# Kernel optimization log

Measured on AMD Instinct MI355X. Metric: run time of the kernel, lower is better.

The kernel has to match this reference:

```python
import jax, jax.numpy as jnp
import numpy as np

B = 512
EPS = 1e-5


def _coords():
    # cvt_coord(i) = [(i//5 - 2)/2, (i%5 - 2)/2] on a 5x5 grid
    c = np.array([[(i // 5 - 2) / 2.0, (i % 5 - 2) / 2.0] for i in range(25)], dtype=np.float32)
    return jnp.asarray(c)  # [25, 2]


def setup_inputs() -> dict:
    key = jax.random.key(0)
    ks = jax.random.split(key, 32)
    d = {
        'img': jax.random.normal(ks[0], (B, 3, 75, 75), jnp.float32),
        'qst': jax.random.normal(ks[1], (B, 11), jnp.float32),
    }
    # conv backbone params
    cin = [3, 24, 24, 24]
    for l in range(4):
        d[f'conv_w{l+1}'] = jax.random.normal(ks[2 + l], (24, cin[l], 3, 3), jnp.float32) * 0.1
        d[f'conv_b{l+1}'] = jnp.zeros((24,), jnp.float32)
        d[f'bn_g{l+1}'] = 1.0 + 0.05 * jax.random.normal(ks[6 + l], (24,), jnp.float32)
        d[f'bn_b{l+1}'] = 0.05 * jax.random.normal(ks[10 + l], (24,), jnp.float32)
    # g MLP (63->256, 256->256 x3)
    d['g_w1'] = jax.random.normal(ks[14], (256, 63), jnp.float32) * 0.05
    d['g_b1'] = jnp.zeros((256,), jnp.float32)
    for l in (2, 3, 4):
        d[f'g_w{l}'] = jax.random.normal(ks[13 + l], (256, 256), jnp.float32) * 0.05
        d[f'g_b{l}'] = jnp.zeros((256,), jnp.float32)
    # f MLP and output head
    d['f_w1'] = jax.random.normal(ks[20], (256, 256), jnp.float32) * 0.05
    d['f_b1'] = jnp.zeros((256,), jnp.float32)
    d['fc2_w'] = jax.random.normal(ks[21], (256, 256), jnp.float32) * 0.05
    d['fc2_b'] = jnp.zeros((256,), jnp.float32)
    d['fc3_w'] = jax.random.normal(ks[22], (10, 256), jnp.float32) * 0.05
    d['fc3_b'] = jnp.zeros((10,), jnp.float32)
    return d


def _conv_bn(x, w, b, g, be):
    y = jax.lax.conv_general_dilated(x, w, (2, 2), [(1, 1), (1, 1)],
                                     dimension_numbers=('NCHW', 'OIHW', 'NCHW'))
    y = jax.nn.relu(y + b[None, :, None, None])
    # BatchNorm2d with batch statistics (training-mode forward)
    mu = jnp.mean(y, axis=(0, 2, 3), keepdims=True)
    var = jnp.var(y, axis=(0, 2, 3), keepdims=True)
    return (y - mu) * jax.lax.rsqrt(var + EPS) * g[None, :, None, None] + be[None, :, None, None]


def _lin(x, w, b):
    return x @ w.T + b


def reference(img, qst,
              conv_w1, conv_b1, bn_g1, bn_b1,
              conv_w2, conv_b2, bn_g2, bn_b2,
              conv_w3, conv_b3, bn_g3, bn_b3,
              conv_w4, conv_b4, bn_g4, bn_b4,
              g_w1, g_b1, g_w2, g_b2, g_w3, g_b3, g_w4, g_b4,
              f_w1, f_b1, fc2_w, fc2_b, fc3_w, fc3_b):
    x = _conv_bn(img, conv_w1, conv_b1, bn_g1, bn_b1)
    x = _conv_bn(x, conv_w2, conv_b2, bn_g2, bn_b2)
    x = _conv_bn(x, conv_w3, conv_b3, bn_g3, bn_b3)
    x = _conv_bn(x, conv_w4, conv_b4, bn_g4, bn_b4)  # [B, 24, 5, 5]
    mb = x.shape[0]
    x_flat = x.reshape(mb, 24, 25).transpose(0, 2, 1)  # [B, 25, 24]
    coords = jnp.broadcast_to(_coords()[None], (mb, 25, 2))
    x_flat = jnp.concatenate([x_flat, coords], axis=2)  # [B, 25, 26]
    # all-pairs: pair (p, q) -> concat(obj_q, obj_p, qst)
    xj = jnp.concatenate([x_flat, jnp.broadcast_to(qst[:, None, :], (mb, 25, 11))], axis=2)  # [B,25,37]
    x_i = jnp.broadcast_to(x_flat[:, None, :, :], (mb, 25, 25, 26))
    x_j = jnp.broadcast_to(xj[:, :, None, :], (mb, 25, 25, 37))
    x_full = jnp.concatenate([x_i, x_j], axis=3).reshape(mb * 625, 63)
    h = jax.nn.relu(_lin(x_full, g_w1, g_b1))
    h = jax.nn.relu(_lin(h, g_w2, g_b2))
    h = jax.nn.relu(_lin(h, g_w3, g_b3))
    h = jax.nn.relu(_lin(h, g_w4, g_b4))
    x_g = h.reshape(mb, 625, 256).sum(axis=1)  # [B, 256]
    x_f = jax.nn.relu(_lin(x_g, f_w1, f_b1))
    x_f = jax.nn.relu(_lin(x_f, fc2_w, fc2_b))  # (dropout omitted: eval/deterministic)
    logits = _lin(x_f, fc3_w, fc3_b)
    return jax.nn.log_softmax(logits, axis=-1)
```

## Files before the change

### kernel.cpp

```cpp
#include <hip/hip_runtime.h>
#include <hip/hip_bf16.h>

#define EPS 1e-5f

typedef _Float16 half_t;
typedef __attribute__((ext_vector_type(8))) _Float16 h16x8;
typedef __attribute__((ext_vector_type(4))) _Float16 h16x4;
typedef __attribute__((ext_vector_type(4))) float f32x4;

__device__ __forceinline__ float relu_f(float x) { return x > 0.f ? x : 0.f; }

#define OFF_Y1   0
#define OFF_Y2   17743872
#define OFF_Y3   22179840
#define OFF_Y4   23408640
#define OFF_ST   23715840
#define OFF_WHL  23718912
#define OFF_A    0
#define OFF_BV   3276800
#define OFF_XG   6553600

__global__ __launch_bounds__(256) void k_prep(const float* w2, const float* w3,
                                              const float* w4, half_t* whl, float* stats) {
    int idx = blockIdx.x * 256 + threadIdx.x;
    if (idx < 3072) stats[idx] = 0.f;
    int l = idx >> 16, e = idx & 65535;
    const float* w = (l == 0) ? w2 : (l == 1) ? w3 : w4;
    float v = w[e];
    int c = e >> 8, k = e & 255;
    int o = ((c >> 4) * 8 + (k >> 5)) * 512 + ((k >> 3) & 3) * 128 + (c & 15) * 8 + (k & 7);
    whl[l * 65536 + o] = (half_t)v;
}

__global__ __launch_bounds__(256, 2) void k_conv1(const float* img, const float* w,
                                                  const float* bias, half_t* y1, float* ostats) {
    __shared__ float wl[648], bl[24], red[4][48];
    int tid = threadIdx.x;
    if (tid < 24) bl[tid] = bias[tid];
    for (int i = tid; i < 648; i += 256) wl[i] = w[i];
    __syncthreads();
    int idx = blockIdx.x * 256 + tid;
    int b2 = idx / 1444, rem = idx % 1444;
    int b0 = b2 * 2;
    int oh = rem / 38, ow = rem % 38;
    float acc0[24], acc1[24];
#pragma unroll
    for (int o = 0; o < 24; ++o) { acc0[o] = bl[o]; acc1[o] = bl[o]; }
    for (int ic = 0; ic < 3; ++ic) {
        float p0[9], p1[9];
#pragma unroll
        for (int kh = 0; kh < 3; ++kh) {
            int ih = oh * 2 - 1 + kh;
#pragma unroll
            for (int kw = 0; kw < 3; ++kw) {
                int iw = ow * 2 - 1 + kw;
                bool ok = (unsigned)ih < 75u && (unsigned)iw < 75u;
                p0[kh * 3 + kw] = ok ? img[((b0 * 3 + ic) * 75 + ih) * 75 + iw] : 0.f;
                p1[kh * 3 + kw] = ok ? img[(((b0 + 1) * 3 + ic) * 75 + ih) * 75 + iw] : 0.f;
            }
        }
#pragma unroll
        for (int o = 0; o < 24; ++o)
#pragma unroll
            for (int t = 0; t < 9; ++t) {
                float wv = wl[(o * 3 + ic) * 9 + t];
                acc0[o] += wv * p0[t];
                acc1[o] += wv * p1[t];
            }
    }
#pragma unroll
    for (int o = 0; o < 24; ++o) { acc0[o] = relu_f(acc0[o]); acc1[o] = relu_f(acc1[o]); }
#pragma unroll
    for (int g = 0; g < 3; ++g) {
        h16x8 a, c;
#pragma unroll
        for (int j = 0; j < 8; ++j) { a[j] = (half_t)acc0[g * 8 + j]; c[j] = (half_t)acc1[g * 8 + j]; }
        *(h16x8*)&y1[((long)(b0) * 1444 + rem) * 24 + g * 8] = a;
        *(h16x8*)&y1[((long)(b0 + 1) * 1444 + rem) * 24 + g * 8] = c;
    }
    int wave = tid >> 6;
#pragma unroll
    for (int o = 0; o < 24; ++o) {
        float v = acc0[o] + acc1[o];
        float v2 = acc0[o] * acc0[o] + acc1[o] * acc1[o];
#pragma unroll
        for (int off = 1; off < 64; off <<= 1) { v += __shfl_xor(v, off); v2 += __shfl_xor(v2, off); }
        if ((tid & 63) == 0) { red[wave][o] = v; red[wave][24 + o] = v2; }
    }
    __syncthreads();
    if (tid < 48)
        atomicAdd(&ostats[(blockIdx.x & 15) * 48 + tid],
                  red[0][tid] + red[1][tid] + red[2][tid] + red[3][tid]);
}

__global__ __launch_bounds__(256) void k_conv2(const half_t* yin, const float* w,
                                               const float* bias, const float* instats,
                                               const float* bng, const float* bnb,
                                               float* yout, float* ostats) {
    __shared__ float wl[5184], bl[24], scs[24], shs[24], red[4][48];
    int tid = threadIdx.x;
    if (tid < 24) {
        float s = 0.f, s2 = 0.f;
#pragma unroll
        for (int k = 0; k < 16; ++k) { s += instats[k * 48 + tid]; s2 += instats[k * 48 + 24 + tid]; }
        float mu = s * (1.f / 739328.f);
        float var = s2 * (1.f / 739328.f) - mu * mu;
        float sca = bng[tid] * rsqrtf(var + EPS);
        scs[tid] = sca; shs[tid] = bnb[tid] - mu * sca;
        bl[tid] = bias[tid];
    }
    for (int i = tid; i < 5184; i += 256) {
        int t = i / 576, r = i % 576;
        int o = r / 24, ic = r % 24;
        wl[i] = w[(o * 24 + ic) * 9 + t];
    }
    __syncthreads();
    int idx = blockIdx.x * 256 + tid;
    int b2 = idx / 361, rem = idx % 361;
    int b0 = b2 * 2;
    int oh = rem / 19, ow = rem % 19;
    float acc0[24], acc1[24];
#pragma unroll
    for (int o = 0; o < 24; ++o) { acc0[o] = bl[o]; acc1[o] = bl[o]; }
#pragma unroll
    for (int kh = 0; kh < 3; ++kh) {
        int ih = oh * 2 - 1 + kh;
#pragma unroll
        for (int kw = 0; kw < 3; ++kw) {
            int iw = ow * 2 - 1 + kw;
            if ((unsigned)ih < 38u && (unsigned)iw < 38u) {
                long px = (long)ih * 38 + iw;
                const half_t* s0 = &yin[((long)b0 * 1444 + px) * 24];
                const half_t* s1 = &yin[((long)(b0 + 1) * 1444 + px) * 24];
                const float* wt = &wl[(kh * 3 + kw) * 576];
#pragma unroll
                for (int g = 0; g < 3; ++g) {
                    h16x8 v0 = *(const h16x8*)&s0[g * 8];
                    h16x8 v1 = *(const h16x8*)&s1[g * 8];
                    float p0[8], p1[8];
#pragma unroll
                    for (int j = 0; j < 8; ++j) {
                        float sc = scs[g * 8 + j], sh = shs[g * 8 + j];
                        p0[j] = (float)v0[j] * sc + sh;
                        p1[j] = (float)v1[j] * sc + sh;
                    }
#pragma unroll
                    for (int o = 0; o < 24; ++o) {
                        const float4* w4 = (const float4*)&wt[o * 24 + g * 8];
                        float4 wa = w4[0], wb = w4[1];
                        acc0[o] += wa.x * p0[0] + wa.y * p0[1] + wa.z * p0[2] + wa.w * p0[3]
                                 + wb.x * p0[4] + wb.y * p0[5] + wb.z * p0[6] + wb.w * p0[7];
                        acc1[o] += wa.x * p1[0] + wa.y * p1[1] + wa.z * p1[2] + wa.w * p1[3]
                                 + wb.x * p1[4] + wb.y * p1[5] + wb.z * p1[6] + wb.w * p1[7];
                    }
                }
            }
        }
    }
    int wave = tid >> 6;
#pragma unroll
    for (int o = 0; o < 24; ++o) {
        acc0[o] = relu_f(acc0[o]);
        acc1[o] = relu_f(acc1[o]);
        yout[(b0 * 24 + o) * 361 + rem] = acc0[o];
        yout[((b0 + 1) * 24 + o) * 361 + rem] = acc1[o];
        float v = acc0[o] + acc1[o];
        float v2 = acc0[o] * acc0[o] + acc1[o] * acc1[o];
#pragma unroll
        for (int off = 1; off < 64; off <<= 1) { v += __shfl_xor(v, off); v2 += __shfl_xor(v2, off); }
        if ((tid & 63) == 0) { red[wave][o] = v; red[wave][24 + o] = v2; }
    }
    __syncthreads();
    if (tid < 48)
        atomicAdd(&ostats[(blockIdx.x & 15) * 48 + tid],
                  red[0][tid] + red[1][tid] + red[2][tid] + red[3][tid]);
}

__global__ __launch_bounds__(256) void k_conv(const float* yin, const float* w,
                                              const float* bias, const float* instats,
                                              const float* bng, const float* bnb,
                                              float* yout, float* ostats,
                                              int Hin, int Hout, float invN) {
    __shared__ float wl[5184], bl[24], sc[24], sh[24], red[4][48];
    int tid = threadIdx.x;
    if (tid < 24) {
        float s = 0.f, s2 = 0.f;
#pragma unroll
        for (int k = 0; k < 16; ++k) { s += instats[k * 48 + tid]; s2 += instats[k * 48 + 24 + tid]; }
        float mu = s * invN;
        float var = s2 * invN - mu * mu;
        float sca = bng[tid] * rsqrtf(var + EPS);
        sc[tid] = sca; sh[tid] = bnb[tid] - mu * sca;
        bl[tid] = bias[tid];
    }
    for (int i = tid; i < 5184; i += 256) wl[i] = w[i];
    __syncthreads();
    int idx = blockIdx.x * 256 + tid;
    int HWo = Hout * Hout;
    int b = idx / HWo, rem = idx % HWo;
    int oh = rem / Hout, ow = rem % Hout;
    float acc[24];
#pragma unroll
    for (int o = 0; o < 24; ++o) acc[o] = bl[o];
    for (int ic = 0; ic < 24; ++ic) {
        float patch[9];
        float scc = sc[ic], shc = sh[ic];
#pragma unroll
        for (int kh = 0; kh < 3; ++kh) {
            int ih = oh * 2 - 1 + kh;
#pragma unroll
            for (int kw = 0; kw < 3; ++kw) {
                int iw = ow * 2 - 1 + kw;
                bool ok = (unsigned)ih < (unsigned)Hin && (unsigned)iw < (unsigned)Hin;
                patch[kh * 3 + kw] = ok ? yin[((b * 24 + ic) * Hin + ih) * Hin + iw] * scc + shc : 0.f;
            }
        }
#pragma unroll
        for (int o = 0; o < 24; ++o)
#pragma unroll
            for (int t = 0; t < 9; ++t) acc[o] += wl[(o * 24 + ic) * 9 + t] * patch[t];
    }
    int wave = tid >> 6;
#pragma unroll
    for (int o = 0; o < 24; ++o) {
        acc[o] = relu_f(acc[o]);
        yout[(b * 24 + o) * HWo + rem] = acc[o];
        float v = acc[o], v2 = v * v;
#pragma unroll
        for (int off = 1; off < 64; off <<= 1) { v += __shfl_xor(v, off); v2 += __shfl_xor(v2, off); }
        if ((tid & 63) == 0) { red[wave][o] = v; red[wave][24 + o] = v2; }
    }
    __syncthreads();
    if (tid < 48)
        atomicAdd(&ostats[(blockIdx.x & 15) * 48 + tid],
                  red[0][tid] + red[1][tid] + red[2][tid] + red[3][tid]);
}

__global__ __launch_bounds__(256) void k_obj(const float* y4, const float* qst,
                                             const float* w1, const float* b1,
                                             const float* instats, const float* bng,
                                             const float* bnb, float* A, float* Bv, float* xg) {
    int b = blockIdx.x, tid = threadIdx.x;
    __shared__ float w1l[16128];
    __shared__ float objs[25][28];
    __shared__ float sc[24], sh[24], q[11];
    xg[b * 256 + tid] = 0.f;
    for (int i = tid; i < 16128; i += 256) w1l[i] = w1[i];
    if (tid < 24) {
        float s = 0.f, s2 = 0.f;
#pragma unroll
        for (int k = 0; k < 16; ++k) { s += instats[k * 48 + tid]; s2 += instats[k * 48 + 24 + tid]; }
        float mu = s * (1.f / 12800.f);
        float var = s2 * (1.f / 12800.f) - mu * mu;
        float sca = bng[tid] * rsqrtf(var + EPS);
        sc[tid] = sca; sh[tid] = bnb[tid] - mu * sca;
    }
    if (tid < 11) q[tid] = qst[b * 11 + tid];
    __syncthreads();
    for (int i = tid; i < 600; i += 256) {
        int c = i / 25, p = i % 25;
        objs[p][c] = y4[b * 600 + i] * sc[c] + sh[c];
    }
    if (tid < 25) { objs[tid][24] = ((tid / 5) - 2) * 0.5f; objs[tid][25] = ((tid % 5) - 2) * 0.5f; }
    __syncthreads();
    float wr[63];
#pragma unroll
    for (int k = 0; k < 63; ++k) wr[k] = w1l[tid * 63 + k];
    float qdot = b1[tid];
#pragma unroll
    for (int j = 0; j < 11; ++j) qdot += wr[52 + j] * q[j];
#pragma unroll 1
    for (int p = 0; p < 25; ++p) {
        float a = 0.f, bv = qdot;
#pragma unroll
        for (int k = 0; k < 26; ++k) { a += wr[k] * objs[p][k]; bv += wr[26 + k] * objs[p][k]; }
        A[(b * 25 + p) * 256 + tid] = a;
        Bv[(b * 25 + p) * 256 + tid] = bv;
    }
}

__global__ __launch_bounds__(256, 4) void k_g(const float* A, const float* Bv, const half_t* whl,
                                              const float* gb2, const float* gb3,
                                              const float* gb4, float* xg) {
    __shared__ alignas(16) half_t h[64 * 264];
    __shared__ float biasL[3][256];
    int tid = threadIdx.x;
    int lb = (blockIdx.x & 7) * 640 + (blockIdx.x >> 3);
    int b = lb / 10, t = lb % 10;
    int r0 = t * 64;
    int rmax = 625 - r0; if (rmax > 64) rmax = 64;
    biasL[0][tid] = gb2[tid];
    biasL[1][tid] = gb3[tid];
    biasL[2][tid] = gb4[tid];
    const float* Ab = A + b * 6400;
    const float* Bb = Bv + b * 6400;
#pragma unroll
    for (int it = 0; it < 16; ++it) {
        int r = it * 4 + (tid >> 6);
        int rs = __builtin_amdgcn_readfirstlane(r);
        int pr = r0 + rs; if (pr > 624) pr = 624;
        int i = pr % 25, j = pr / 25;
        int c4 = (tid & 63) << 2;
        float4 av = *(const float4*)&Ab[i * 256 + c4];
        float4 bv = *(const float4*)&Bb[j * 256 + c4];
        h16x4 hv = {(half_t)relu_f(av.x + bv.x), (half_t)relu_f(av.y + bv.y),
                    (half_t)relu_f(av.z + bv.z), (half_t)relu_f(av.w + bv.w)};
        *(h16x4*)&h[r * 264 + c4] = hv;
    }
    __syncthreads();
    int cg = tid >> 6, lane = tid & 63;
    int quad = lane >> 4, l15 = lane & 15;
    const half_t* hr = h + l15 * 264;
    const half_t* Wl = whl + (cg * 4) * 8 * 512 + lane * 8;
#pragma unroll 1
    for (int layer = 0; layer < 3; ++layer) {
        const half_t* W = Wl + layer * 65536;
        f32x4 acc[4][4];
#pragma unroll
        for (int mi = 0; mi < 4; ++mi)
#pragma unroll
            for (int nt = 0; nt < 4; ++nt) acc[mi][nt] = (f32x4){0.f, 0.f, 0.f, 0.f};
        h16x8 aw0 = *(const h16x8*)&W[0 * 4096];
        h16x8 aw1 = *(const h16x8*)&W[1 * 4096];
        h16x8 aw2 = *(const h16x8*)&W[2 * 4096];
        h16x8 aw3 = *(const h16x8*)&W[3 * 4096];
        h16x8 bh0 = *(const h16x8*)&hr[0 * 4224 + quad * 8];
        h16x8 bh1 = *(const h16x8*)&hr[1 * 4224 + quad * 8];
#pragma unroll 2
        for (int ks = 0; ks < 8; ++ks) {
            int ko = ks * 32 + quad * 8;
            int ksn = (ks + 1) & 7;
            int kon = ksn * 32 + quad * 8;
            h16x8 bh2 = *(const h16x8*)&hr[2 * 4224 + ko];
            h16x8 bh3 = *(const h16x8*)&hr[3 * 4224 + ko];
            h16x8 an0 = *(const h16x8*)&W[0 * 4096 + ksn * 512];
            h16x8 an1 = *(const h16x8*)&W[1 * 4096 + ksn * 512];
            h16x8 an2 = *(const h16x8*)&W[2 * 4096 + ksn * 512];
            h16x8 an3 = *(const h16x8*)&W[3 * 4096 + ksn * 512];
            __builtin_amdgcn_s_setprio(1);
            acc[0][0] = __builtin_amdgcn_mfma_f32_16x16x32_f16(aw0, bh0, acc[0][0], 0, 0, 0);
            acc[1][0] = __builtin_amdgcn_mfma_f32_16x16x32_f16(aw1, bh0, acc[1][0], 0, 0, 0);
            acc[2][0] = __builtin_amdgcn_mfma_f32_16x16x32_f16(aw2, bh0, acc[2][0], 0, 0, 0);
            acc[3][0] = __builtin_amdgcn_mfma_f32_16x16x32_f16(aw3, bh0, acc[3][0], 0, 0, 0);
            acc[0][1] = __builtin_amdgcn_mfma_f32_16x16x32_f16(aw0, bh1, acc[0][1], 0, 0, 0);
            acc[1][1] = __builtin_amdgcn_mfma_f32_16x16x32_f16(aw1, bh1, acc[1][1], 0, 0, 0);
            acc[2][1] = __builtin_amdgcn_mfma_f32_16x16x32_f16(aw2, bh1, acc[2][1], 0, 0, 0);
            acc[3][1] = __builtin_amdgcn_mfma_f32_16x16x32_f16(aw3, bh1, acc[3][1], 0, 0, 0);
            h16x8 bn0 = *(const h16x8*)&hr[0 * 4224 + kon];
            h16x8 bn1 = *(const h16x8*)&hr[1 * 4224 + kon];
            acc[0][2] = __builtin_amdgcn_mfma_f32_16x16x32_f16(aw0, bh2, acc[0][2], 0, 0, 0);
            acc[1][2] = __builtin_amdgcn_mfma_f32_16x16x32_f16(aw1, bh2, acc[1][2], 0, 0, 0);
            acc[2][2] = __builtin_amdgcn_mfma_f32_16x16x32_f16(aw2, bh2, acc[2][2], 0, 0, 0);
            acc[3][2] = __builtin_amdgcn_mfma_f32_16x16x32_f16(aw3, bh2, acc[3][2], 0, 0, 0);
            acc[0][3] = __builtin_amdgcn_mfma_f32_16x16x32_f16(aw0, bh3, acc[0][3], 0, 0, 0);
            acc[1][3] = __builtin_amdgcn_mfma_f32_16x16x32_f16(aw1, bh3, acc[1][3], 0, 0, 0);
            acc[2][3] = __builtin_amdgcn_mfma_f32_16x16x32_f16(aw2, bh3, acc[2][3], 0, 0, 0);
            acc[3][3] = __builtin_amdgcn_mfma_f32_16x16x32_f16(aw3, bh3, acc[3][3], 0, 0, 0);
            __builtin_amdgcn_s_setprio(0);
            aw0 = an0; aw1 = an1; aw2 = an2; aw3 = an3;
            bh0 = bn0; bh1 = bn1;
        }
        __syncthreads();
        if (layer < 2) {
#pragma unroll
            for (int mi = 0; mi < 4; ++mi) {
                int c0 = cg * 64 + mi * 16 + quad * 4;
#pragma unroll
                for (int nt = 0; nt < 4; ++nt) {
                    int row = nt * 16 + l15;
                    h16x4 hv;
#pragma unroll
                    for (int v = 0; v < 4; ++v)
                        hv[v] = (half_t)relu_f(acc[mi][nt][v] + biasL[layer][c0 + v]);
                    *(h16x4*)&h[row * 264 + c0] = hv;
                }
            }
            __syncthreads();
        } else {
#pragma unroll
            for (int mi = 0; mi < 4; ++mi) {
                int c0 = cg * 64 + mi * 16 + quad * 4;
#pragma unroll
                for (int v = 0; v < 4; ++v) {
                    float s = 0.f;
#pragma unroll
                    for (int nt = 0; nt < 4; ++nt) {
                        int row = nt * 16 + l15;
                        float x = relu_f(acc[mi][nt][v] + biasL[2][c0 + v]);
                        if (row < rmax) s += x;
                    }
                    s += __shfl_xor(s, 1);
                    s += __shfl_xor(s, 2);
                    s += __shfl_xor(s, 4);
                    s += __shfl_xor(s, 8);
                    if (l15 == 0) atomicAdd(&xg[b * 256 + c0 + v], s);
                }
            }
        }
    }
}

__global__ __launch_bounds__(256) void k_f(const float* xg, const float* fw1, const float* fb1,
                                           const float* fw2, const float* fb2,
                                           const float* fw3, const float* fb3, float* out) {
    int b0 = blockIdx.x * 2, tid = threadIdx.x;
    __shared__ float xb[2][256], h1[2][256], l10[2][10], red[2];
    xb[0][tid] = xg[b0 * 256 + tid];
    xb[1][tid] = xg[(b0 + 1) * 256 + tid];
    __syncthreads();
    float s0 = fb1[tid], s1 = s0;
    {
        const float4* wr = (const float4*)&fw1[tid * 256];
        const float4* x0 = (const float4*)xb[0];
        const float4* x1 = (const float4*)xb[1];
#pragma unroll 8
        for (int k = 0; k < 64; ++k) {
            float4 w = wr[k], a = x0[k], c = x1[k];
            s0 += w.x * a.x + w.y * a.y + w.z * a.z + w.w * a.w;
            s1 += w.x * c.x + w.y * c.y + w.z * c.z + w.w * c.w;
        }
    }
    h1[0][tid] = relu_f(s0);
    h1[1][tid] = relu_f(s1);
    __syncthreads();
    s0 = fb2[tid]; s1 = s0;
    {
        const float4* wr = (const float4*)&fw2[tid * 256];
        const float4* x0 = (const float4*)h1[0];
        const float4* x1 = (const float4*)h1[1];
#pragma unroll 8
        for (int k = 0; k < 64; ++k) {
            float4 w = wr[k], a = x0[k], c = x1[k];
            s0 += w.x * a.x + w.y * a.y + w.z * a.z + w.w * a.w;
            s1 += w.x * c.x + w.y * c.y + w.z * c.z + w.w * c.w;
        }
    }
    __syncthreads();
    xb[0][tid] = relu_f(s0);
    xb[1][tid] = relu_f(s1);
    __syncthreads();
    if (tid < 20) {
        int bb = tid / 10, o = tid % 10;
        float v = fb3[o];
        const float4* wr = (const float4*)&fw3[o * 256];
        const float4* hv = (const float4*)xb[bb];
#pragma unroll 8
        for (int k = 0; k < 64; ++k) {
            float4 w = wr[k], x = hv[k];
            v += w.x * x.x + w.y * x.y + w.z * x.z + w.w * x.w;
        }
        l10[bb][o] = v;
    }
    __syncthreads();
    if (tid < 2) {
        float m = l10[tid][0];
        for (int i = 1; i < 10; ++i) m = fmaxf(m, l10[tid][i]);
        float e = 0.f;
        for (int i = 0; i < 10; ++i) e += expf(l10[tid][i] - m);
        red[tid] = m + logf(e);
    }
    __syncthreads();
    if (tid < 20) {
        int bb = tid / 10, o = tid % 10;
        out[(b0 + bb) * 10 + o] = l10[bb][o] - red[bb];
    }
}

extern "C" void kernel_launch(void* const* d_in, const int* in_sizes, int n_in,
                              void* d_out, int out_size, void* d_ws, size_t ws_size,
                              hipStream_t stream) {
    const float* img = (const float*)d_in[0];
    const float* qst = (const float*)d_in[1];
    const float* cw[4] = {(const float*)d_in[2], (const float*)d_in[6],
                          (const float*)d_in[10], (const float*)d_in[14]};
    const float* cb[4] = {(const float*)d_in[3], (const float*)d_in[7],
                          (const float*)d_in[11], (const float*)d_in[15]};
    const float* bg[4] = {(const float*)d_in[4], (const float*)d_in[8],
                          (const float*)d_in[12], (const float*)d_in[16]};
    const float* bb[4] = {(const float*)d_in[5], (const float*)d_in[9],
                          (const float*)d_in[13], (const float*)d_in[17]};
    const float* gw1 = (const float*)d_in[18];
    const float* gb1 = (const float*)d_in[19];
    const float* gw2 = (const float*)d_in[20];
    const float* gb2 = (const float*)d_in[21];
    const float* gw3 = (const float*)d_in[22];
    const float* gb3 = (const float*)d_in[23];
    const float* gw4 = (const float*)d_in[24];
    const float* gb4 = (const float*)d_in[25];
    const float* fw1 = (const float*)d_in[26];
    const float* fb1 = (const float*)d_in[27];
    const float* fw2 = (const float*)d_in[28];
    const float* fb2 = (const float*)d_in[29];
    const float* fw3 = (const float*)d_in[30];
    const float* fb3 = (const float*)d_in[31];

    float* ws = (float*)d_ws;
    half_t* y1 = (half_t*)(ws + OFF_Y1);
    float* y2 = ws + OFF_Y2;
    float* y3 = ws + OFF_Y3;
    float* y4 = ws + OFF_Y4;
    float* st = ws + OFF_ST;
    half_t* whl = (half_t*)(ws + OFF_WHL);
    float* A = ws + OFF_A;
    float* Bv = ws + OFF_BV;
    float* xg = ws + OFF_XG;
    float* out = (float*)d_out;

    k_prep<<<768, 256, 0, stream>>>(gw2, gw3, gw4, whl, st);
    k_conv1<<<1444, 256, 0, stream>>>(img, cw[0], cb[0], y1, st + 0 * 768);
    k_conv2<<<361, 256, 0, stream>>>(y1, cw[1], cb[1], st + 0 * 768, bg[0], bb[0], y2,
                                     st + 1 * 768);
    k_conv<<<200, 256, 0, stream>>>(y2, cw[2], cb[2], st + 1 * 768, bg[1], bb[1], y3,
                                    st + 2 * 768, 19, 10, 1.f / 184832.f);
    k_conv<<<50, 256, 0, stream>>>(y3, cw[3], cb[3], st + 2 * 768, bg[2], bb[2], y4,
                                   st + 3 * 768, 10, 5, 1.f / 51200.f);
    k_obj<<<512, 256, 0, stream>>>(y4, qst, gw1, gb1, st + 3 * 768, bg[3], bb[3], A, Bv, xg);
    k_g<<<5120, 256, 0, stream>>>(A, Bv, whl, gb2, gb3, gb4, xg);
    k_f<<<256, 256, 0, stream>>>(xg, fw1, fb1, fw2, fb2, fw3, fb3, out);
}
```

Measured before the change: 583.2 us.

## Rewrite conv2 as per-image implicit GEMM on MFMA with LDS-staged input

```diff
diff --git a/kernel.cpp b/kernel.cpp
--- a/kernel.cpp
+++ b/kernel.cpp
@@ -19,6 +19,7 @@
 #define OFF_A    0
 #define OFF_BV   3276800
 #define OFF_XG   6553600
+#define OFF_WHL2 8871936
 
 __global__ __launch_bounds__(256) void k_prep(const float* w2, const float* w3,
                                               const float* w4, half_t* whl, float* stats) {
@@ -32,6 +33,21 @@
     whl[l * 65536 + o] = (half_t)v;
 }
 
+__global__ __launch_bounds__(256) void k_prep2(const float* w2, half_t* whl2) {
+    int idx = blockIdx.x * 256 + threadIdx.x;
+    int ntile = idx / 3584, r = idx % 3584;
+    int ks = r / 512, w = r % 512;
+    int quad = w / 128, l15 = (w >> 3) & 15, j = w & 7;
+    int k = ks * 32 + quad * 8 + j;
+    int oc = ntile * 16 + l15;
+    float v = 0.f;
+    if (k < 216 && oc < 24) {
+        int tap = k / 24, ic = k % 24;
+        v = w2[(oc * 24 + ic) * 9 + tap];
+    }
+    whl2[idx] = (half_t)v;
+}
+
 __global__ __launch_bounds__(256, 2) void k_conv1(const float* img, const float* w,
                                                   const float* bias, half_t* y1, float* ostats) {
     __shared__ float wl[648], bl[24], red[4][48];
@@ -93,12 +109,16 @@
                   red[0][tid] + red[1][tid] + red[2][tid] + red[3][tid]);
 }
 
-__global__ __launch_bounds__(256) void k_conv2(const half_t* yin, const float* w,
+__global__ __launch_bounds__(256) void k_conv2(const half_t* yin, const half_t* whl2,
                                                const float* bias, const float* instats,
                                                const float* bng, const float* bnb,
                                                float* yout, float* ostats) {
-    __shared__ float wl[5184], bl[24], scs[24], shs[24], red[4][48];
+    __shared__ half_t yL[34672];
+    __shared__ half_t wf[7168];
+    __shared__ float outL[8856];
+    __shared__ float scs[24], shs[24], bl[24], red[4][48];
     int tid = threadIdx.x;
+    int b = blockIdx.x;
     if (tid < 24) {
         float s = 0.f, s2 = 0.f;
 #pragma unroll
@@ -109,68 +129,75 @@
         scs[tid] = sca; shs[tid] = bnb[tid] - mu * sca;
         bl[tid] = bias[tid];
     }
-    for (int i = tid; i < 5184; i += 256) {
-        int t = i / 576, r = i % 576;
-        int o = r / 24, ic = r % 24;
-        wl[i] = w[(o * 24 + ic) * 9 + t];
-    }
-    __syncthreads();
-    int idx = blockIdx.x * 256 + tid;
-    int b2 = idx / 361, rem = idx % 361;
-    int b0 = b2 * 2;
-    int oh = rem / 19, ow = rem % 19;
-    float acc0[24], acc1[24];
-#pragma unroll
-    for (int o = 0; o < 24; ++o) { acc0[o] = bl[o]; acc1[o] = bl[o]; }
-#pragma unroll
-    for (int kh = 0; kh < 3; ++kh) {
-        int ih = oh * 2 - 1 + kh;
-#pragma unroll
-        for (int kw = 0; kw < 3; ++kw) {
-            int iw = ow * 2 - 1 + kw;
-            if ((unsigned)ih < 38u && (unsigned)iw < 38u) {
-                long px = (long)ih * 38 + iw;
-                const half_t* s0 = &yin[((long)b0 * 1444 + px) * 24];
-                const half_t* s1 = &yin[((long)(b0 + 1) * 1444 + px) * 24];
-                const float* wt = &wl[(kh * 3 + kw) * 576];
-#pragma unroll
-                for (int g = 0; g < 3; ++g) {
-                    h16x8 v0 = *(const h16x8*)&s0[g * 8];
-                    h16x8 v1 = *(const h16x8*)&s1[g * 8];
-                    float p0[8], p1[8];
-#pragma unroll
-                    for (int j = 0; j < 8; ++j) {
-                        float sc = scs[g * 8 + j], sh = shs[g * 8 + j];
-                        p0[j] = (float)v0[j] * sc + sh;
-                        p1[j] = (float)v1[j] * sc + sh;
-                    }
-#pragma unroll
-                    for (int o = 0; o < 24; ++o) {
-                        const float4* w4 = (const float4*)&wt[o * 24 + g * 8];
-                        float4 wa = w4[0], wb = w4[1];
-                        acc0[o] += wa.x * p0[0] + wa.y * p0[1] + wa.z * p0[2] + wa.w * p0[3]
-                                 + wb.x * p0[4] + wb.y * p0[5] + wb.z * p0[6] + wb.w * p0[7];
-                        acc1[o] += wa.x * p1[0] + wa.y * p1[1] + wa.z * p1[2] + wa.w * p1[3]
-                                 + wb.x * p1[4] + wb.y * p1[5] + wb.z * p1[6] + wb.w * p1[7];
-                    }
-                }
+    if (tid < 16) yL[34656 + tid] = (half_t)0.f;
+    for (int i = tid; i < 896; i += 256)
+        ((h16x8*)wf)[i] = ((const h16x8*)whl2)[i];
+    __syncthreads();
+    const half_t* ybase = yin + (long)b * 34656;
+    for (int i = tid; i < 4332; i += 256) {
+        h16x8 v = *(const h16x8*)&ybase[i * 8];
+        int ch0 = (i % 3) * 8;
+        h16x8 o;
+#pragma unroll
+        for (int j = 0; j < 8; ++j)
+            o[j] = (half_t)((float)v[j] * scs[ch0 + j] + shs[ch0 + j]);
+        *(h16x8*)&yL[i * 8] = o;
+    }
+    __syncthreads();
+    int wv = tid >> 6, lane = tid & 63, quad = lane >> 4, l15 = lane & 15;
+    float bb0 = bl[l15];
+    float bb1 = (l15 < 8) ? bl[16 + l15] : 0.f;
+    float s0 = 0.f, q0 = 0.f, s1 = 0.f, q1 = 0.f;
+    int t0 = wv * 6, t1 = t0 + 6; if (t1 > 23) t1 = 23;
+#pragma unroll 1
+    for (int t = t0; t < t1; ++t) {
+        int px0 = t * 16;
+        int pxa = px0 + l15; if (pxa > 360) pxa = 360;
+        int oh = pxa / 19, ow = pxa % 19;
+        f32x4 a0 = (f32x4){0.f, 0.f, 0.f, 0.f};
+        f32x4 a1 = (f32x4){0.f, 0.f, 0.f, 0.f};
+#pragma unroll
+        for (int ks = 0; ks < 7; ++ks) {
+            int k0 = ks * 32 + quad * 8;
+            int tap = k0 / 24, ic0 = k0 - tap * 24;
+            int kh = tap / 3, kw = tap - kh * 3;
+            int ih = oh * 2 - 1 + kh, iw = ow * 2 - 1 + kw;
+            bool val = (tap < 9) && ((unsigned)ih < 38u) && ((unsigned)iw < 38u);
+            int aoff = val ? ((ih * 38 + iw) * 24 + ic0) : 34656;
+            h16x8 af = *(const h16x8*)&yL[aoff];
+            h16x8 w0 = *(const h16x8*)&wf[ks * 512 + quad * 128 + l15 * 8];
+            h16x8 w1 = *(const h16x8*)&wf[3584 + ks * 512 + quad * 128 + l15 * 8];
+            a0 = __builtin_amdgcn_mfma_f32_16x16x32_f16(af, w0, a0, 0, 0, 0);
+            a1 = __builtin_amdgcn_mfma_f32_16x16x32_f16(af, w1, a1, 0, 0, 0);
+        }
+#pragma unroll
+        for (int v = 0; v < 4; ++v) {
+            int p = px0 + quad * 4 + v;
+            bool pv = p < 361;
+            float x0 = relu_f(a0[v] + bb0);
+            float x1 = relu_f(a1[v] + bb1);
+            outL[l15 * 369 + p] = x0;
+            if (l15 < 8) outL[(16 + l15) * 369 + p] = x1;
+            if (pv) {
+                s0 += x0; q0 += x0 * x0;
+                if (l15 < 8) { s1 += x1; q1 += x1 * x1; }
             }
         }
     }
-    int wave = tid >> 6;
-#pragma unroll
-    for (int o = 0; o < 24; ++o) {
-        acc0[o] = relu_f(acc0[o]);
-        acc1[o] = relu_f(acc1[o]);
-        yout[(b0 * 24 + o) * 361 + rem] = acc0[o];
-        yout[((b0 + 1) * 24 + o) * 361 + rem] = acc1[o];
-        float v = acc0[o] + acc1[o];
-        float v2 = acc0[o] * acc0[o] + acc1[o] * acc1[o];
-#pragma unroll
-        for (int off = 1; off < 64; off <<= 1) { v += __shfl_xor(v, off); v2 += __shfl_xor(v2, off); }
-        if ((tid & 63) == 0) { red[wave][o] = v; red[wave][24 + o] = v2; }
-    }
-    __syncthreads();
+    s0 += __shfl_xor(s0, 16); s0 += __shfl_xor(s0, 32);
+    q0 += __shfl_xor(q0, 16); q0 += __shfl_xor(q0, 32);
+    s1 += __shfl_xor(s1, 16); s1 += __shfl_xor(s1, 32);
+    q1 += __shfl_xor(q1, 16); q1 += __shfl_xor(q1, 32);
+    if (quad == 0) {
+        red[wv][l15] = s0; red[wv][24 + l15] = q0;
+        if (l15 < 8) { red[wv][16 + l15] = s1; red[wv][40 + l15] = q1; }
+    }
+    __syncthreads();
+    float* yo = yout + (long)b * 8664;
+    for (int i = tid; i < 8664; i += 256) {
+        int oc = i / 361, p = i - oc * 361;
+        yo[i] = outL[oc * 369 + p];
+    }
     if (tid < 48)
         atomicAdd(&ostats[(blockIdx.x & 15) * 48 + tid],
                   red[0][tid] + red[1][tid] + red[2][tid] + red[3][tid]);
@@ -501,14 +528,16 @@
     float* y4 = ws + OFF_Y4;
     float* st = ws + OFF_ST;
     half_t* whl = (half_t*)(ws + OFF_WHL);
+    half_t* whl2 = (half_t*)(ws + OFF_WHL2);
     float* A = ws + OFF_A;
     float* Bv = ws + OFF_BV;
     float* xg = ws + OFF_XG;
     float* out = (float*)d_out;
 
     k_prep<<<768, 256, 0, stream>>>(gw2, gw3, gw4, whl, st);
+    k_prep2<<<28, 256, 0, stream>>>(cw[1], whl2);
     k_conv1<<<1444, 256, 0, stream>>>(img, cw[0], cb[0], y1, st + 0 * 768);
-    k_conv2<<<361, 256, 0, stream>>>(y1, cw[1], cb[1], st + 0 * 768, bg[0], bb[0], y2,
+    k_conv2<<<512, 256, 0, stream>>>(y1, whl2, cb[1], st + 0 * 768, bg[0], bb[0], y2,
                                      st + 1 * 768);
     k_conv<<<200, 256, 0, stream>>>(y2, cw[2], cb[2], st + 1 * 768, bg[1], bb[1], y3,
                                     st + 2 * 768, 19, 10, 1.f / 184832.f);
```

After: 521.7 us. 1.12x faster.
